# Kernel tuning notes

Hardware: AMD Instinct MI355X
Metric: run time of the kernel (lower is better)

## Reference

```python
import jax, jax.numpy as jnp
import numpy as np

NUM_STEPS = 32
BETA = 0.9
THRESHOLD = 1.0   # LIF firing threshold
LAT_THR = 0.01    # snntorch spikegen.latency default threshold
EPS = 1e-7        # snntorch epsilon
SLOPE = 25.0      # fast_sigmoid surrogate slope
ENC_THR = 0.75    # SpikeEncoder latency_threshold

B, S, F_IN = 512, 64, 128
HIDDEN = [256, 256, 128]


def spike_fn(u):
    # Heaviside forward; surrogate grad handled in fwdbwd module. Forward-only here.
    return (u > 0).astype(u.dtype)


def latency_encode(x, num_steps):
    """SpikeEncoder('latency') -> snntorch.spikegen.latency, normalize=True, linear=False."""
    # gate small values
    x = jnp.where(x < ENC_THR, jnp.zeros_like(x), x)
    # per-channel min-max normalization over the sequence dim (dim=1)
    x_min = jnp.min(x, axis=1, keepdims=True)
    x_max = jnp.max(x, axis=1, keepdims=True)
    xn = (x - x_min) / (x_max - x_min + 1e-8)
    # logarithmic latency code (tau=1, first_spike_time=0, normalize=True)
    d = jnp.clip(xn, LAT_THR + EPS, None)
    t = jnp.log(d / (d - LAT_THR))
    t_max = np.log((LAT_THR + EPS) / EPS)  # spike time of smallest intensity
    t = t * (num_steps - 1) / np.float32(t_max)
    t_idx = jnp.clip(jnp.round(t), 0, num_steps - 1).astype(jnp.int32)  # (B,S,F)
    # one-hot over time -> (T, B, S, F), matches spikegen scatter
    steps = jnp.arange(num_steps, dtype=jnp.int32).reshape(-1, 1, 1, 1)
    return (steps == t_idx[None]).astype(jnp.float32)


def snn_block(x, W, b, beta, thr):
    """Linear over all timesteps, then LIF (reset-by-subtraction) via scan.
    x: (T, B, in) -> spk: (T, B, hidden)"""
    cur = jnp.einsum('tbi,hi->tbh', x, W) + b

    def step(mem, c):
        # snntorch Leaky: reset computed from previous mem (detached)
        reset = jax.lax.stop_gradient((mem - thr > 0).astype(mem.dtype))
        mem = beta * mem + c - reset * thr
        spk = spike_fn(mem - thr)
        return mem, spk

    mem0 = jnp.zeros(cur.shape[1:], cur.dtype)
    _, spk = jax.lax.scan(step, cur[0] * 0 + mem0, cur)
    return spk


def setup_inputs() -> dict:
    key = jax.random.key(0)
    ks = jax.random.split(key, 7)
    x = jax.random.normal(ks[0], (B, S, F_IN), dtype=jnp.float32)
    sizes = [F_IN] + HIDDEN
    params = {}
    for i in range(3):
        fan_in = sizes[i]
        bound = 1.0 / np.sqrt(fan_in)
        params[f'W{i+1}'] = jax.random.uniform(ks[2 * i + 1], (sizes[i + 1], fan_in),
                                               minval=-bound, maxval=bound, dtype=jnp.float32)
        params[f'b{i+1}'] = jax.random.uniform(ks[2 * i + 2], (sizes[i + 1],),
                                               minval=-bound, maxval=bound, dtype=jnp.float32)
    return {'x': x, **params}


def reference(x, W1, b1, W2, b2, W3, b3):
    spikes = latency_encode(x, NUM_STEPS)        # (T, B, S, F)
    spikes = spikes.mean(axis=2)                 # (T, B, F)
    spikes = snn_block(spikes, W1, b1, BETA, THRESHOLD)
    spikes = snn_block(spikes, W2, b2, BETA, THRESHOLD)
    spikes = snn_block(spikes, W3, b3, BETA, THRESHOLD)
    return spikes                                # (T, B, hidden_sizes[-1])
```

## Files before the change

### kernel.cpp

```cpp
#include <hip/hip_runtime.h>
#include <cstddef>

#define T_STEPS 32
#define B_SZ    512
#define S_SZ    64
#define F_INPUT 128
#define H1      256
#define H2      256
#define H3      128

typedef _Float16 half_t;
typedef __attribute__((ext_vector_type(8))) _Float16 half8;
typedef __attribute__((ext_vector_type(4))) float   float4v;

__device__ inline void split_store_sw(float w, half_t* out, int n, int k, int kchunks) {
    half_t hi = (half_t)w;
    float hif = (float)hi;
    if (fabsf(hif) < 6.103515625e-05f) { hi = (half_t)0.0f; hif = 0.0f; }
    half_t lo = (half_t)((w - hif) * 4096.0f);
    int n_tile = n >> 4, lr = n & 15;
    int k_chunk = k >> 5, kin = k & 31, quad = kin >> 3, j = kin & 7;
    size_t base = (size_t)(n_tile * kchunks + k_chunk) * 1024;
    size_t off  = base + (size_t)((quad << 4) + lr) * 8 + j;
    out[off]       = hi;
    out[off + 512] = lo;
}

__global__ __launch_bounds__(256)
void prep_w_kernel(const float* __restrict__ W1, const float* __restrict__ W2,
                   const float* __restrict__ W3,
                   half_t* __restrict__ ws1, half_t* __restrict__ ws2,
                   half_t* __restrict__ ws3) {
    int e = blockIdx.x * blockDim.x + threadIdx.x;
    if (e < H1 * F_INPUT) {
        split_store_sw(W1[e], ws1, e / F_INPUT, e % F_INPUT, F_INPUT / 32);
    } else if (e < H1 * F_INPUT + H2 * H1) {
        int i = e - H1 * F_INPUT;
        split_store_sw(W2[i], ws2, i / H1, i % H1, H1 / 32);
    } else {
        int i = e - H1 * F_INPUT - H2 * H1;
        split_store_sw(W3[i], ws3, i / H2, i % H2, H2 / 32);
    }
}

#define CUR_STRIDE 260
#define AS_STRIDE  136
#define SPK_STRIDE 264
#define SMEM_CUR   0
#define SMEM_AS    33280
#define SMEM_SPK   33280
#define SMEM_TOTAL 50176

template<int KCHUNKS, int NT, int ASTRIDE>
__device__ __forceinline__ void gemm_phase(const half_t* __restrict__ Wsw,
                                           const float*  __restrict__ bias,
                                           const half_t* __restrict__ Als,
                                           float* __restrict__ curT,
                                           int wave, int lane) {
    const int quad = lane >> 4, lr = lane & 15;
    float4v acc_h[2][NT], acc_l[2][NT];
#pragma unroll
    for (int mt = 0; mt < 2; ++mt)
#pragma unroll
        for (int nt = 0; nt < NT; ++nt) {
            acc_h[mt][nt] = (float4v){0.0f, 0.0f, 0.0f, 0.0f};
            acc_l[mt][nt] = (float4v){0.0f, 0.0f, 0.0f, 0.0f};
        }

    half8 wh[NT], wl[NT];
#pragma unroll
    for (int nt = 0; nt < NT; ++nt) {
        const half_t* p = Wsw + ((size_t)(wave * NT + nt) * KCHUNKS) * 1024 + lane * 8;
        wh[nt] = *(const half8*)(p);
        wl[nt] = *(const half8*)(p + 512);
    }

#pragma unroll
    for (int c = 0; c < KCHUNKS; ++c) {
        half8 a0 = *(const half8*)(Als + lr * ASTRIDE        + c * 32 + quad * 8);
        half8 a1 = *(const half8*)(Als + (16 + lr) * ASTRIDE + c * 32 + quad * 8);
        half8 nwh[NT], nwl[NT];
        if (c + 1 < KCHUNKS) {
#pragma unroll
            for (int nt = 0; nt < NT; ++nt) {
                const half_t* p =
                    Wsw + ((size_t)(wave * NT + nt) * KCHUNKS + c + 1) * 1024 + lane * 8;
                nwh[nt] = *(const half8*)(p);
                nwl[nt] = *(const half8*)(p + 512);
            }
        }
#pragma unroll
        for (int nt = 0; nt < NT; ++nt) {
            acc_h[0][nt] = __builtin_amdgcn_mfma_f32_16x16x32_f16(a0, wh[nt], acc_h[0][nt], 0, 0, 0);
            acc_h[1][nt] = __builtin_amdgcn_mfma_f32_16x16x32_f16(a1, wh[nt], acc_h[1][nt], 0, 0, 0);
            acc_l[0][nt] = __builtin_amdgcn_mfma_f32_16x16x32_f16(a0, wl[nt], acc_l[0][nt], 0, 0, 0);
            acc_l[1][nt] = __builtin_amdgcn_mfma_f32_16x16x32_f16(a1, wl[nt], acc_l[1][nt], 0, 0, 0);
        }
#pragma unroll
        for (int nt = 0; nt < NT; ++nt) { wh[nt] = nwh[nt]; wl[nt] = nwl[nt]; }
    }

#pragma unroll
    for (int nt = 0; nt < NT; ++nt) {
        int col = wave * NT * 16 + nt * 16 + lr;
        float bj = bias[col];
#pragma unroll
        for (int mt = 0; mt < 2; ++mt) {
            int rbase = mt * 16 + quad * 4;
#pragma unroll
            for (int r = 0; r < 4; ++r) {
                float v = acc_h[mt][nt][r] + 2.44140625e-04f * acc_l[mt][nt][r];
                curT[(rbase + r) * CUR_STRIDE + col] = v + bj;
            }
        }
    }
}

__global__ __launch_bounds__(512, 4)
void snn_mega_kernel(const float* __restrict__ x,
                     const half_t* __restrict__ ws1, const float* __restrict__ b1,
                     const half_t* __restrict__ ws2, const float* __restrict__ b2,
                     const half_t* __restrict__ ws3, const float* __restrict__ b3,
                     float* __restrict__ out) {
    __shared__ __align__(16) char smem[SMEM_TOTAL];
    float*  curT = (float*) (smem + SMEM_CUR);
    half_t* As   = (half_t*)(smem + SMEM_AS);
    half_t* spk  = (half_t*)(smem + SMEM_SPK);

    const int tid  = threadIdx.x;
    const int b    = blockIdx.x;
    const int wave = tid >> 6;
    const int lane = tid & 63;

    const int f  = tid & 127;
    const int sh = (tid >> 7) & 1;
    const float* xp = x + (size_t)b * (S_SZ * F_INPUT) + (size_t)sh * 32 * F_INPUT + f;
    float* scratch = curT;

    float v[32];
    if (tid < 256) {
#pragma unroll
        for (int s = 0; s < 32; ++s) {
            float val = xp[(size_t)s * F_INPUT];
            v[s] = (val < 0.75f) ? 0.0f : val;
        }
        float mn = 1e30f, mx = -1e30f;
#pragma unroll
        for (int s = 0; s < 32; ++s) {
            mn = fminf(mn, v[s]);
            mx = fmaxf(mx, v[s]);
        }
        scratch[sh * 128 + f]       = mn;
        scratch[256 + sh * 128 + f] = mx;
    }
    __syncthreads();
    float fmn = fminf(scratch[f], scratch[128 + f]);
    float fmx = fmaxf(scratch[256 + f], scratch[384 + f]);
    __syncthreads();

    if (tid < 256) {
        float* hist = scratch;
#pragma unroll
        for (int t = 0; t < T_STEPS; ++t) hist[sh * 4096 + t * 128 + f] = 0.0f;
        const float denom = fmx - fmn + 1e-8f;
#pragma unroll
        for (int s = 0; s < 32; ++s) {
            float g = v[s];
            float xn = (g - fmn) / denom;
            float d  = fmaxf(xn, 0.0100001f);
            float tt = logf(d / (d - 0.01f));
            tt = tt * 31.0f;
            tt = tt / 11.512935464920229f;
            float tr = rintf(tt);
            tr = fminf(fmaxf(tr, 0.0f), 31.0f);
            hist[sh * 4096 + (int)tr * 128 + f] += 1.0f;
        }
    }
    __syncthreads();

#pragma unroll
    for (int i = 0; i < 8; ++i) {
        int idx = tid + i * 512;
        int t = idx >> 7, ff = idx & 127;
        float cnt = scratch[t * 128 + ff] + scratch[4096 + t * 128 + ff];
        As[t * AS_STRIDE + ff] = (half_t)(cnt * 0.015625f);
    }
    __syncthreads();

    gemm_phase<F_INPUT / 32, 2, AS_STRIDE>(ws1, b1, As, curT, wave, lane);
    __syncthreads();
    if (tid < 256) {
#pragma clang fp contract(off)
        const int h = tid;
        float mem = 0.0f;
#pragma unroll
        for (int t = 0; t < T_STEPS; ++t) {
            float c = curT[t * CUR_STRIDE + h];
            float reset = (mem - 1.0f > 0.0f) ? 1.0f : 0.0f;
            float p = 0.9f * mem;
            p = p + c;
            mem = p - reset;
            spk[t * SPK_STRIDE + h] = (half_t)((mem - 1.0f > 0.0f) ? 1.0f : 0.0f);
        }
    }
    __syncthreads();

    gemm_phase<H1 / 32, 2, SPK_STRIDE>(ws2, b2, spk, curT, wave, lane);
    __syncthreads();
    if (tid < 256) {
#pragma clang fp contract(off)
        const int h = tid;
        float mem = 0.0f;
#pragma unroll
        for (int t = 0; t < T_STEPS; ++t) {
            float c = curT[t * CUR_STRIDE + h];
            float reset = (mem - 1.0f > 0.0f) ? 1.0f : 0.0f;
            float p = 0.9f * mem;
            p = p + c;
            mem = p - reset;
            spk[t * SPK_STRIDE + h] = (half_t)((mem - 1.0f > 0.0f) ? 1.0f : 0.0f);
        }
    }
    __syncthreads();

    gemm_phase<H2 / 32, 1, SPK_STRIDE>(ws3, b3, spk, curT, wave, lane);
    __syncthreads();
    if (tid < H3) {
#pragma clang fp contract(off)
        const int h = tid;
        float mem = 0.0f;
#pragma unroll
        for (int t = 0; t < T_STEPS; ++t) {
            float c = curT[t * CUR_STRIDE + h];
            float reset = (mem - 1.0f > 0.0f) ? 1.0f : 0.0f;
            float p = 0.9f * mem;
            p = p + c;
            mem = p - reset;
            out[((size_t)t * B_SZ + b) * H3 + h] = (mem - 1.0f > 0.0f) ? 1.0f : 0.0f;
        }
    }
}

extern "C" void kernel_launch(void* const* d_in, const int* in_sizes, int n_in,
                              void* d_out, int out_size, void* d_ws, size_t ws_size,
                              hipStream_t stream) {
    const float* x  = (const float*)d_in[0];
    const float* W1 = (const float*)d_in[1];
    const float* b1 = (const float*)d_in[2];
    const float* W2 = (const float*)d_in[3];
    const float* b2 = (const float*)d_in[4];
    const float* W3 = (const float*)d_in[5];
    const float* b3 = (const float*)d_in[6];
    float* out = (float*)d_out;

    char* ws = (char*)d_ws;
    half_t* ws1 = (half_t*)ws;
    half_t* ws2 = (half_t*)(ws + 128 * 1024);
    half_t* ws3 = (half_t*)(ws + 384 * 1024);

    prep_w_kernel<<<(H1 * F_INPUT + H2 * H1 + H3 * H2) / 256, 256, 0, stream>>>(
        W1, W2, W3, ws1, ws2, ws3);

    snn_mega_kernel<<<B_SZ, 512, 0, stream>>>(x, ws1, b1, ws2, b2, ws3, b3, out);
}
```

Before: 98.86 us.

## Prefetch first weight chunks early and spread encoding across all threads

```diff
diff --git a/kernel.cpp b/kernel.cpp
--- a/kernel.cpp
+++ b/kernel.cpp
@@ -51,12 +51,27 @@
 #define SMEM_SPK   33280
 #define SMEM_TOTAL 50176
 
-template<int KCHUNKS, int NT, int ASTRIDE>
+template<int KCHUNKS, int NT>
+__device__ __forceinline__ void preload_w(const half_t* __restrict__ Wsw,
+                                          int wave, int lane,
+                                          half8* __restrict__ ph,
+                                          half8* __restrict__ pl) {
+#pragma unroll
+    for (int nt = 0; nt < NT; ++nt) {
+        const half_t* p = Wsw + ((size_t)(wave * NT + nt) * KCHUNKS) * 1024 + lane * 8;
+        ph[nt] = *(const half8*)(p);
+        pl[nt] = *(const half8*)(p + 512);
+    }
+}
+
+template<int KCHUNKS, int NT, int ASTRIDE, bool PRE>
 __device__ __forceinline__ void gemm_phase(const half_t* __restrict__ Wsw,
                                            const float*  __restrict__ bias,
                                            const half_t* __restrict__ Als,
                                            float* __restrict__ curT,
-                                           int wave, int lane) {
+                                           int wave, int lane,
+                                           const half8* __restrict__ pre_h,
+                                           const half8* __restrict__ pre_l) {
     const int quad = lane >> 4, lr = lane & 15;
     float4v acc_h[2][NT], acc_l[2][NT];
 #pragma unroll
@@ -68,11 +83,16 @@
         }
 
     half8 wh[NT], wl[NT];
-#pragma unroll
-    for (int nt = 0; nt < NT; ++nt) {
-        const half_t* p = Wsw + ((size_t)(wave * NT + nt) * KCHUNKS) * 1024 + lane * 8;
-        wh[nt] = *(const half8*)(p);
-        wl[nt] = *(const half8*)(p + 512);
+    if constexpr (PRE) {
+#pragma unroll
+        for (int nt = 0; nt < NT; ++nt) { wh[nt] = pre_h[nt]; wl[nt] = pre_l[nt]; }
+    } else {
+#pragma unroll
+        for (int nt = 0; nt < NT; ++nt) {
+            const half_t* p = Wsw + ((size_t)(wave * NT + nt) * KCHUNKS) * 1024 + lane * 8;
+            wh[nt] = *(const half8*)(p);
+            wl[nt] = *(const half8*)(p + 512);
+        }
     }
 
 #pragma unroll
@@ -132,49 +152,48 @@
     const int wave = tid >> 6;
     const int lane = tid & 63;
 
+    half8 w1h[2], w1l[2];
+    preload_w<F_INPUT / 32, 2>(ws1, wave, lane, w1h, w1l);
+
     const int f  = tid & 127;
-    const int sh = (tid >> 7) & 1;
-    const float* xp = x + (size_t)b * (S_SZ * F_INPUT) + (size_t)sh * 32 * F_INPUT + f;
-    float* scratch = curT;
-
-    float v[32];
-    if (tid < 256) {
-#pragma unroll
-        for (int s = 0; s < 32; ++s) {
-            float val = xp[(size_t)s * F_INPUT];
-            v[s] = (val < 0.75f) ? 0.0f : val;
-        }
-        float mn = 1e30f, mx = -1e30f;
-#pragma unroll
-        for (int s = 0; s < 32; ++s) {
-            mn = fminf(mn, v[s]);
-            mx = fmaxf(mx, v[s]);
-        }
-        scratch[sh * 128 + f]       = mn;
-        scratch[256 + sh * 128 + f] = mx;
-    }
-    __syncthreads();
-    float fmn = fminf(scratch[f], scratch[128 + f]);
-    float fmx = fmaxf(scratch[256 + f], scratch[384 + f]);
-    __syncthreads();
-
-    if (tid < 256) {
-        float* hist = scratch;
-#pragma unroll
-        for (int t = 0; t < T_STEPS; ++t) hist[sh * 4096 + t * 128 + f] = 0.0f;
-        const float denom = fmx - fmn + 1e-8f;
-#pragma unroll
-        for (int s = 0; s < 32; ++s) {
-            float g = v[s];
-            float xn = (g - fmn) / denom;
-            float d  = fmaxf(xn, 0.0100001f);
-            float tt = logf(d / (d - 0.01f));
-            tt = tt * 31.0f;
-            tt = tt / 11.512935464920229f;
-            float tr = rintf(tt);
-            tr = fminf(fmaxf(tr, 0.0f), 31.0f);
-            hist[sh * 4096 + (int)tr * 128 + f] += 1.0f;
-        }
+    const int sq = tid >> 7;
+    const float* xp = x + (size_t)b * (S_SZ * F_INPUT) + (size_t)(sq * 16) * F_INPUT + f;
+    float* hist  = curT;
+    float* mpart = (float*)(smem + SMEM_AS);
+
+    float v[16];
+#pragma unroll
+    for (int s = 0; s < 16; ++s) {
+        float val = xp[(size_t)s * F_INPUT];
+        v[s] = (val < 0.75f) ? 0.0f : val;
+    }
+    float mn = 1e30f, mx = -1e30f;
+#pragma unroll
+    for (int s = 0; s < 16; ++s) {
+        mn = fminf(mn, v[s]);
+        mx = fmaxf(mx, v[s]);
+    }
+    mpart[sq * 128 + f]       = mn;
+    mpart[512 + sq * 128 + f] = mx;
+#pragma unroll
+    for (int i = 0; i < 8; ++i) hist[tid + i * 512] = 0.0f;
+    __syncthreads();
+
+    float fmn = fminf(fminf(mpart[f],       mpart[128 + f]),
+                      fminf(mpart[256 + f], mpart[384 + f]));
+    float fmx = fmaxf(fmaxf(mpart[512 + f], mpart[640 + f]),
+                      fmaxf(mpart[768 + f], mpart[896 + f]));
+    const float denom = fmx - fmn + 1e-8f;
+#pragma unroll
+    for (int s = 0; s < 16; ++s) {
+        float xn = (v[s] - fmn) / denom;
+        float d  = fmaxf(xn, 0.0100001f);
+        float tt = logf(d / (d - 0.01f));
+        tt = tt * 31.0f;
+        tt = tt / 11.512935464920229f;
+        float tr = rintf(tt);
+        tr = fminf(fmaxf(tr, 0.0f), 31.0f);
+        atomicAdd(&hist[(int)tr * 128 + f], 1.0f);
     }
     __syncthreads();
 
@@ -182,13 +201,14 @@
     for (int i = 0; i < 8; ++i) {
         int idx = tid + i * 512;
         int t = idx >> 7, ff = idx & 127;
-        float cnt = scratch[t * 128 + ff] + scratch[4096 + t * 128 + ff];
-        As[t * AS_STRIDE + ff] = (half_t)(cnt * 0.015625f);
-    }
-    __syncthreads();
-
-    gemm_phase<F_INPUT / 32, 2, AS_STRIDE>(ws1, b1, As, curT, wave, lane);
-    __syncthreads();
+        As[t * AS_STRIDE + ff] = (half_t)(hist[idx] * 0.015625f);
+    }
+    __syncthreads();
+
+    gemm_phase<F_INPUT / 32, 2, AS_STRIDE, true>(ws1, b1, As, curT, wave, lane, w1h, w1l);
+    __syncthreads();
+    half8 w2h[2], w2l[2];
+    preload_w<H1 / 32, 2>(ws2, wave, lane, w2h, w2l);
     if (tid < 256) {
 #pragma clang fp contract(off)
         const int h = tid;
@@ -205,8 +225,10 @@
     }
     __syncthreads();
 
-    gemm_phase<H1 / 32, 2, SPK_STRIDE>(ws2, b2, spk, curT, wave, lane);
-    __syncthreads();
+    gemm_phase<H1 / 32, 2, SPK_STRIDE, true>(ws2, b2, spk, curT, wave, lane, w2h, w2l);
+    __syncthreads();
+    half8 w3h[1], w3l[1];
+    preload_w<H2 / 32, 1>(ws3, wave, lane, w3h, w3l);
     if (tid < 256) {
 #pragma clang fp contract(off)
         const int h = tid;
@@ -223,7 +245,7 @@
     }
     __syncthreads();
 
-    gemm_phase<H2 / 32, 1, SPK_STRIDE>(ws3, b3, spk, curT, wave, lane);
+    gemm_phase<H2 / 32, 1, SPK_STRIDE, true>(ws3, b3, spk, curT, wave, lane, w3h, w3l);
     __syncthreads();
     if (tid < H3) {
 #pragma clang fp contract(off)
```

After: 112.1 us. 13.4% more time.
